# Optimization experiments

Hardware: AMD Instinct MI355X
Metric: run time of the kernel (lower is better)

Reference implementation:

```python
import jax, jax.numpy as jnp
import numpy as np

FH = FW = 3          # field_height, field_width
SF = 2               # scale_factor passed to set_transforms
NODES = 32           # out_channels
D_IN = 16            # in_channels (field depth)
HID = 32             # mlpnodes[0]; mlpnodes = [32, 1]


def maxpool_3x3_s2_p1(x):
    # Deterministic stand-in for FractionalMaxPool2d(kernel=3, output=(H//2, W//2)):
    return jax.lax.reduce_window(
        x, -jnp.inf, jax.lax.max,
        window_dimensions=(1, 1, 3, 3),
        window_strides=(1, 1, 2, 2),
        padding=((0, 0), (0, 0), (1, 1), (1, 1)))


def unfold_3x3(x):
    # torch.nn.Unfold(kernel=(3,3), padding=1): (N,D,H,W) -> (N, D, 9, H*W)
    N, D, H, W = x.shape
    xp = jnp.pad(x, ((0, 0), (0, 0), (1, 1), (1, 1)))
    patches = jnp.stack([xp[:, :, i:i + H, j:j + W]
                         for i in range(3) for j in range(3)], axis=2)
    return patches.reshape(N, D, 9, H * W)


def setup_inputs() -> dict:
    key = jax.random.key(0)
    k = jax.random.split(key, 6)
    N, H, W = 32, 96, 96
    x = jax.random.normal(k[0], (N, D_IN, H, W), dtype=jnp.float32)
    # S per node: xavier_uniform on shape (1, D, 3, 3): fan_in=D*9, fan_out=1*9
    bound_S = float(np.sqrt(6.0 / (D_IN * 9 + 9)))
    S = jax.random.uniform(k[1], (NODES, D_IN, FH, FW), jnp.float32, -bound_S, bound_S)
    # per-node MLP: Linear(D_IN -> HID) -> ReLU -> Linear(HID -> 1) -> ReLU
    b1w = 1.0 / np.sqrt(D_IN)
    W1 = jax.random.uniform(k[2], (NODES, D_IN, HID), jnp.float32, -b1w, b1w)
    b1 = jax.random.uniform(k[3], (NODES, HID), jnp.float32, -b1w, b1w)
    b2w = 1.0 / np.sqrt(HID)
    W2 = jax.random.uniform(k[4], (NODES, HID, 1), jnp.float32, -b2w, b2w)
    b2 = jax.random.uniform(k[5], (NODES, 1), jnp.float32, -b2w, b2w)
    return {"x": x, "S": S, "W1": W1, "b1": b1, "W2": W2, "b2": b2}


def reference(x, S, W1, b1, W2, b2):
    N, D, H, W = x.shape
    Hs, Ws = H // SF, W // SF
    U = unfold_3x3(maxpool_3x3_s2_p1(x))            # (N, D, 9, L), L = Hs*Ws
    Sf = S.reshape(S.shape[0], D, FH * FW)          # (O, D, 9)
    # StructFun: M[n,d,l] = sum_k S[d,k] * U[n,d,k,l], batched over nodes o
    M = jnp.einsum('odk,ndkl->nlod', Sf, U)         # (N, L, O, D)
    # StructBlock: reshape to (N,Hs,Ws,D) then per-node MLP over last dim
    h = jax.nn.relu(jnp.einsum('nlod,odh->nloh', M, W1) + b1)   # (N, L, O, HID)
    y = jax.nn.relu(jnp.einsum('nloh,ohe->nloe', h, W2) + b2)   # (N, L, O, 1)
    out = y[..., 0].reshape(N, Hs, Ws, -1)          # (N, Hs, Ws, O)
    return out.transpose(0, 3, 1, 2)                # (N, O, Hs, Ws)
```

## Files before the change

### kernel.cpp

```cpp
#include <hip/hip_runtime.h>
#include <math.h>

typedef __bf16 bf16;
typedef __bf16 bf16x8 __attribute__((ext_vector_type(8)));
typedef float  f32x16 __attribute__((ext_vector_type(16)));

#define D_INC 16
#define NODES 32
#define HID   32
#define HS    48
#define WSZ   48
#define NPX   (HS*WSZ)
#define H_IN  96
#define W_IN  96
#define N_B   32

#define MP_BLOCKS   1152
#define WPRE_BLOCKS 640

__global__ __launch_bounds__(256) void pre_kernel(
    const float* __restrict__ x, bf16* __restrict__ Pg,
    const float* __restrict__ S, const float* __restrict__ W1,
    const float* __restrict__ b1, bf16* __restrict__ Wp)
{
    if (blockIdx.x < MP_BLOCKS) {
        int idx = blockIdx.x * 256 + threadIdx.x;
        int c  = idx % WSZ;
        int t  = idx / WSZ;
        int q  = t & 3;
        int rr = t >> 2;
        int r  = rr % HS;
        int n  = rr / HS;

        const float* xb = x + ((size_t)(n * D_INC + q * 4)) * (H_IN * W_IN);

        float m0 = -INFINITY, m1 = -INFINITY, m2 = -INFINITY, m3 = -INFINITY;
        #pragma unroll
        for (int dr = 0; dr < 3; ++dr) {
            int xr = 2 * r - 1 + dr;
            if (xr < 0) continue;
            #pragma unroll
            for (int dc = 0; dc < 3; ++dc) {
                int xc = 2 * c - 1 + dc;
                if (xc < 0) continue;
                const float* p = xb + xr * W_IN + xc;
                m0 = fmaxf(m0, p[0 * H_IN * W_IN]);
                m1 = fmaxf(m1, p[1 * H_IN * W_IN]);
                m2 = fmaxf(m2, p[2 * H_IN * W_IN]);
                m3 = fmaxf(m3, p[3 * H_IN * W_IN]);
            }
        }
        union { bf16 hh[4]; uint2 u; } v;
        v.hh[0] = (bf16)m0; v.hh[1] = (bf16)m1; v.hh[2] = (bf16)m2; v.hh[3] = (bf16)m3;
        *(uint2*)(Pg + ((size_t)((n * HS + r) * WSZ + c)) * D_INC + q * 4) = v.u;
    } else {
        int idx = (blockIdx.x - MP_BLOCKS) * 256 + threadIdx.x;
        if (idx >= NODES * 10 * 2 * HID * 8) return;
        int j  = idx & 7;
        int h  = (idx >> 3) & 31;
        int qp = (idx >> 8) & 1;
        int os = idx >> 9;
        int s  = os % 10;
        int o  = os / 10;
        int k  = 16 * s + 8 * qp + j;
        float v = 0.f;
        if (k < 144) {
            int t = k >> 4;
            int d = k & 15;
            v = S[(o * D_INC + d) * 9 + t] * W1[(o * D_INC + d) * HID + h];
        } else if (k == 144) {
            v = b1[o * HID + h];
        }
        Wp[idx] = (bf16)v;
    }
}

__global__ __launch_bounds__(256, 2) void gemm_kernel(
    const bf16* __restrict__ Pg, const bf16* __restrict__ Wp,
    const float* __restrict__ W2, const float* __restrict__ b2,
    float* __restrict__ out)
{
    __shared__ __align__(16) bf16 Pl[26 * 2 * 50 * 8];

    const int hb   = blockIdx.x;
    const int n    = blockIdx.y;
    const int ob   = blockIdx.z * 2;
    const int tid  = threadIdx.x;
    const int lane = tid & 63;
    const int w    = tid >> 6;
    const int ln31 = lane & 31;
    const int qp   = lane >> 5;

    const int r0 = hb * 24;

    const uint4 z4 = make_uint4(0u, 0u, 0u, 0u);

    for (int u = tid; u < 26 * 48 * 2; u += 256) {
        int half = u & 1;
        int c    = (u >> 1) % 48;
        int row  = (u >> 1) / 48;
        int pr   = r0 - 1 + row;
        uint4 v  = z4;
        if (pr >= 0 && pr < HS)
            v = *(const uint4*)(Pg + ((size_t)(n * HS + pr) * WSZ + c) * D_INC + half * 8);
        *(uint4*)(Pl + ((row * 2 + half) * 50 + (c + 1)) * 8) = v;
    }
    if (tid < 104) {
        int row  = tid >> 2;
        int half = (tid >> 1) & 1;
        int side = tid & 1;
        *(uint4*)(Pl + ((row * 2 + half) * 50 + side * 49) * 8) = z4;
    }
    __syncthreads();

    bf16x8 Af[2][10];
    #pragma unroll
    for (int e = 0; e < 2; ++e) {
        const bf16* wp = Wp + (size_t)((ob + e) * 10) * 512 + lane * 8;
        #pragma unroll
        for (int s = 0; s < 10; ++s)
            Af[e][s] = *(const bf16x8*)(wp + s * 512);
    }
    float4 w2v[2][4];
    float  bb[2];
    #pragma unroll
    for (int e = 0; e < 2; ++e) {
        const float* w2b = W2 + (ob + e) * HID + 4 * qp;
        w2v[e][0] = *(const float4*)(w2b);
        w2v[e][1] = *(const float4*)(w2b + 8);
        w2v[e][2] = *(const float4*)(w2b + 16);
        w2v[e][3] = *(const float4*)(w2b + 24);
        bb[e] = b2[ob + e];
    }

    const int    p_base   = w * 288 + ln31;
    const size_t outbase0 = (size_t)(n * NODES + ob) * NPX + hb * 1152;

    #pragma unroll
    for (int ti = 0; ti < 9; ++ti) {
        const int p  = p_base + ti * 32;
        const int rl = p / 48;
        const int c  = p - rl * 48;
        const int base_ch = (rl * 2 + qp) * 50 + c;

        bf16x8 Bf[10];
        #pragma unroll
        for (int s = 0; s < 9; ++s) {
            const int di = s / 3, dj = s % 3;
            Bf[s] = *(const bf16x8*)(Pl + (base_ch + di * 100 + dj) * 8);
        }
        {
            bf16x8 bias = {};
            if (qp == 0) bias[0] = (bf16)1.0f;
            Bf[9] = bias;
        }

        f32x16 acc0 = {};
        f32x16 acc1 = {};
        #pragma unroll
        for (int s = 0; s < 10; ++s) {
            acc0 = __builtin_amdgcn_mfma_f32_32x32x16_bf16(Af[0][s], Bf[s], acc0, 0, 0, 0);
            acc1 = __builtin_amdgcn_mfma_f32_32x32x16_bf16(Af[1][s], Bf[s], acc1, 0, 0, 0);
        }

        #pragma unroll
        for (int e = 0; e < 2; ++e) {
            const f32x16 a = e ? acc1 : acc0;
            float part;
            part  = fmaxf(a[0],  0.f) * w2v[e][0].x;
            part  = fmaf(fmaxf(a[1],  0.f), w2v[e][0].y, part);
            part  = fmaf(fmaxf(a[2],  0.f), w2v[e][0].z, part);
            part  = fmaf(fmaxf(a[3],  0.f), w2v[e][0].w, part);
            part  = fmaf(fmaxf(a[4],  0.f), w2v[e][1].x, part);
            part  = fmaf(fmaxf(a[5],  0.f), w2v[e][1].y, part);
            part  = fmaf(fmaxf(a[6],  0.f), w2v[e][1].z, part);
            part  = fmaf(fmaxf(a[7],  0.f), w2v[e][1].w, part);
            part  = fmaf(fmaxf(a[8],  0.f), w2v[e][2].x, part);
            part  = fmaf(fmaxf(a[9],  0.f), w2v[e][2].y, part);
            part  = fmaf(fmaxf(a[10], 0.f), w2v[e][2].z, part);
            part  = fmaf(fmaxf(a[11], 0.f), w2v[e][2].w, part);
            part  = fmaf(fmaxf(a[12], 0.f), w2v[e][3].x, part);
            part  = fmaf(fmaxf(a[13], 0.f), w2v[e][3].y, part);
            part  = fmaf(fmaxf(a[14], 0.f), w2v[e][3].z, part);
            part  = fmaf(fmaxf(a[15], 0.f), w2v[e][3].w, part);
            float tot = part + __shfl_xor(part, 32);
            tot = fmaxf(tot + bb[e], 0.f);
            if (qp == 0)
                out[outbase0 + (size_t)e * NPX + p] = tot;
        }
    }
}

extern "C" void kernel_launch(void* const* d_in, const int* in_sizes, int n_in,
                              void* d_out, int out_size, void* d_ws, size_t ws_size,
                              hipStream_t stream)
{
    const float* x  = (const float*)d_in[0];
    const float* S  = (const float*)d_in[1];
    const float* W1 = (const float*)d_in[2];
    const float* b1 = (const float*)d_in[3];
    const float* W2 = (const float*)d_in[4];
    const float* b2 = (const float*)d_in[5];
    float* out = (float*)d_out;

    bf16* Pg = (bf16*)d_ws;
    bf16* Wp = (bf16*)((char*)d_ws + (size_t)N_B * NPX * D_INC * 2);

    pre_kernel<<<MP_BLOCKS + WPRE_BLOCKS, 256, 0, stream>>>(x, Pg, S, W1, b1, Wp);

    dim3 grid(2, N_B, 16);
    gemm_kernel<<<grid, 256, 0, stream>>>(Pg, Wp, W2, b2, out);
}
```

Measured before the change: 104.6 us.

## Stage input row tiles in LDS for maxpool to cut redundant global reads

```diff
diff --git a/kernel.cpp b/kernel.cpp
--- a/kernel.cpp
+++ b/kernel.cpp
@@ -15,7 +15,7 @@
 #define W_IN  96
 #define N_B   32
 
-#define MP_BLOCKS   1152
+#define MP_BLOCKS   768
 #define WPRE_BLOCKS 640
 
 __global__ __launch_bounds__(256) void pre_kernel(
@@ -23,38 +23,72 @@
     const float* __restrict__ S, const float* __restrict__ W1,
     const float* __restrict__ b1, bf16* __restrict__ Wp)
 {
+    __shared__ float Pt[4][17][97];
+
+    const int tid = threadIdx.x;
+
     if (blockIdx.x < MP_BLOCKS) {
-        int idx = blockIdx.x * 256 + threadIdx.x;
-        int c  = idx % WSZ;
-        int t  = idx / WSZ;
-        int q  = t & 3;
-        int rr = t >> 2;
-        int r  = rr % HS;
-        int n  = rr / HS;
-
-        const float* xb = x + ((size_t)(n * D_INC + q * 4)) * (H_IN * W_IN);
-
-        float m0 = -INFINITY, m1 = -INFINITY, m2 = -INFINITY, m3 = -INFINITY;
-        #pragma unroll
-        for (int dr = 0; dr < 3; ++dr) {
-            int xr = 2 * r - 1 + dr;
-            if (xr < 0) continue;
-            #pragma unroll
-            for (int dc = 0; dc < 3; ++dc) {
-                int xc = 2 * c - 1 + dc;
-                if (xc < 0) continue;
-                const float* p = xb + xr * W_IN + xc;
-                m0 = fmaxf(m0, p[0 * H_IN * W_IN]);
-                m1 = fmaxf(m1, p[1 * H_IN * W_IN]);
-                m2 = fmaxf(m2, p[2 * H_IN * W_IN]);
-                m3 = fmaxf(m3, p[3 * H_IN * W_IN]);
+        const int b  = blockIdx.x;
+        const int rb = b % 6;
+        const int q  = (b / 6) & 3;
+        const int n  = b / 24;
+        const int R0 = 16 * rb - 1;
+
+        const float* xb = x + (size_t)(n * D_INC + q * 4) * (H_IN * W_IN);
+
+        for (int s = tid; s < 4 * 17 * 24; s += 256) {
+            int c4  = s % 24;
+            int t2  = s / 24;
+            int row = t2 % 17;
+            int ch  = t2 / 17;
+            int xr  = R0 + row;
+            float4 v = make_float4(-INFINITY, -INFINITY, -INFINITY, -INFINITY);
+            if (xr >= 0)
+                v = *(const float4*)(xb + (size_t)ch * (H_IN * W_IN) + xr * W_IN + c4 * 4);
+            Pt[ch][row][c4 * 4 + 0] = v.x;
+            Pt[ch][row][c4 * 4 + 1] = v.y;
+            Pt[ch][row][c4 * 4 + 2] = v.z;
+            Pt[ch][row][c4 * 4 + 3] = v.w;
+        }
+        __syncthreads();
+
+        int px = tid;
+        #pragma unroll
+        for (int k = 0; k < 2; ++k, px += 256) {
+            if (px < 384) {
+                int rl = px / 48;
+                int c  = px % 48;
+                int r  = 8 * rb + rl;
+                int row0 = 2 * rl;
+
+                float m[4];
+                #pragma unroll
+                for (int ch = 0; ch < 4; ++ch) {
+                    int cl = 2 * c - 1;
+                    float mm;
+                    {
+                        float a0 = (cl >= 0) ? Pt[ch][row0 + 0][cl] : -INFINITY;
+                        float a1 = (cl >= 0) ? Pt[ch][row0 + 1][cl] : -INFINITY;
+                        float a2 = (cl >= 0) ? Pt[ch][row0 + 2][cl] : -INFINITY;
+                        mm = fmaxf(fmaxf(a0, a1), a2);
+                    }
+                    #pragma unroll
+                    for (int dj = 1; dj < 3; ++dj) {
+                        int cc = 2 * c - 1 + dj;
+                        mm = fmaxf(mm, Pt[ch][row0 + 0][cc]);
+                        mm = fmaxf(mm, Pt[ch][row0 + 1][cc]);
+                        mm = fmaxf(mm, Pt[ch][row0 + 2][cc]);
+                    }
+                    m[ch] = mm;
+                }
+                union { bf16 hh[4]; uint2 u; } v;
+                v.hh[0] = (bf16)m[0]; v.hh[1] = (bf16)m[1];
+                v.hh[2] = (bf16)m[2]; v.hh[3] = (bf16)m[3];
+                *(uint2*)(Pg + ((size_t)((n * HS + r) * WSZ + c)) * D_INC + q * 4) = v.u;
             }
         }
-        union { bf16 hh[4]; uint2 u; } v;
-        v.hh[0] = (bf16)m0; v.hh[1] = (bf16)m1; v.hh[2] = (bf16)m2; v.hh[3] = (bf16)m3;
-        *(uint2*)(Pg + ((size_t)((n * HS + r) * WSZ + c)) * D_INC + q * 4) = v.u;
     } else {
-        int idx = (blockIdx.x - MP_BLOCKS) * 256 + threadIdx.x;
+        int idx = (blockIdx.x - MP_BLOCKS) * 256 + tid;
         if (idx >= NODES * 10 * 2 * HID * 8) return;
         int j  = idx & 7;
         int h  = (idx >> 3) & 31;
```

Result: no change. 103.6 us (-0.9%).
